# Performance work log

Hardware: AMD Instinct MI355X
Metric: run time of the kernel (lower is better)

The kernel has to match this reference:

```python
import jax, jax.numpy as jnp
import numpy as np

H = 1024      # hidden_size
F = 1024      # intermediate_size
E = 8         # num_experts
K = 2         # num_experts_per_tok
B, S = 1, 2048


def setup_inputs() -> dict:
    key = jax.random.key(0)
    ks = jax.random.split(key, 8)
    s = 0.02
    return {
        "hidden_states": jax.random.normal(ks[0], (B, S, H), jnp.float32),
        "w_gate": jax.random.normal(ks[1], (H, E), jnp.float32) * s,
        "w_gate_proj": jax.random.normal(ks[2], (E, H, F), jnp.float32) * s,   # per-expert gate_proj
        "w_up_proj": jax.random.normal(ks[3], (E, H, F), jnp.float32) * s,     # per-expert up_proj
        "w_down_proj": jax.random.normal(ks[4], (E, F, H), jnp.float32) * s,   # per-expert down_proj
        "w_shared_gate": jax.random.normal(ks[5], (H, F), jnp.float32) * s,
        "w_shared_up": jax.random.normal(ks[6], (H, F), jnp.float32) * s,
        "w_shared_down": jax.random.normal(ks[7], (F, H), jnp.float32) * s,
    }


def reference(hidden_states, w_gate, w_gate_proj, w_up_proj, w_down_proj,
              w_shared_gate, w_shared_up, w_shared_down):
    b, s, h = hidden_states.shape
    x = hidden_states.reshape(-1, h)                       # [T, H]
    t = x.shape[0]

    # --- router ---
    router_logits = x @ w_gate                             # [T, E]
    topk_vals, topk_idx = jax.lax.top_k(router_logits, K)  # [T, K]
    expert_weights = jax.nn.softmax(topk_vals.astype(jnp.float32), axis=-1).astype(x.dtype)

    # dense per-token per-expert combine weight [T, E] (zero where not selected)
    combine = jnp.zeros((t, E), x.dtype).at[jnp.arange(t)[:, None], topk_idx].add(expert_weights)

    # --- all experts as one grouped GEMM (weight-zero experts contribute 0) ---
    g = jnp.einsum('th,ehf->tef', x, w_gate_proj)          # [T, E, F]
    u = jnp.einsum('th,ehf->tef', x, w_up_proj)            # [T, E, F]
    y = jnp.einsum('tef,efh->teh', jax.nn.silu(g) * u, w_down_proj)  # [T, E, H]
    out = jnp.einsum('teh,te->th', y, combine)             # [T, H]

    # --- shared expert ---
    shared = (jax.nn.silu(x @ w_shared_gate) * (x @ w_shared_up)) @ w_shared_down
    out = (out + shared).reshape(b, s, h)

    aux_loss = jnp.float32(0.0)
    return out, aux_loss
```

## Files before the change

kernel.cpp:

```cpp
#include <hip/hip_runtime.h>
#include <hip/hip_bf16.h>
#include <stdint.h>

#define HDIM 1024
#define FDIM 1024
#define TTOK 2048
#define CAP  2048
#define MSZ  (1024*1024)

typedef __attribute__((ext_vector_type(8))) __bf16 bf16x8;
typedef __attribute__((ext_vector_type(4))) float  f32x4;

static __device__ __forceinline__ unsigned short f2bf(float v) {
  unsigned int u = __float_as_uint(v);
  u += 0x7FFF + ((u >> 16) & 1);
  return (unsigned short)(u >> 16);
}

static __device__ __forceinline__ unsigned pk2(float a, float b) {
  return (unsigned)f2bf(a) | ((unsigned)f2bf(b) << 16);
}

static __device__ __forceinline__ void gload_lds16(const void* g, void* l) {
  __builtin_amdgcn_global_load_lds(
      (const __attribute__((address_space(1))) unsigned int*)g,
      (__attribute__((address_space(3))) unsigned int*)l, 16, 0, 0);
}


__global__ __launch_bounds__(256) void k_prep(
    const float* __restrict__ x, const float* __restrict__ wg,
    const float* __restrict__ wgp, const float* __restrict__ wsg,
    const float* __restrict__ wup, const float* __restrict__ wsu,
    const float* __restrict__ wdp, const float* __restrict__ wsd,
    unsigned short* __restrict__ wB, unsigned short* __restrict__ xb,
    int* __restrict__ counts, int* __restrict__ tok_id, float* __restrict__ tok_w,
    int2* __restrict__ tsl, float* __restrict__ tw) {
  int b = blockIdx.x;
  int tid = threadIdx.x;
  if (b < 512) {
    int t = (b << 2) + (tid >> 6);
    int L = tid & 63;
    const float* xr = x + (size_t)t * HDIM;
    float acc[8] = {0, 0, 0, 0, 0, 0, 0, 0};
    for (int h = L; h < HDIM; h += 64) {
      float xv = xr[h];
      const float* wr = wg + h * 8;
      #pragma unroll
      for (int e = 0; e < 8; e++) acc[e] += xv * wr[e];
    }
    #pragma unroll
    for (int e = 0; e < 8; e++) {
      float v = acc[e];
      for (int off = 32; off > 0; off >>= 1) v += __shfl_xor(v, off);
      acc[e] = v;
    }
    if (L == 0) {
      int i1 = 0; float v1 = acc[0];
      #pragma unroll
      for (int e = 1; e < 8; e++) if (acc[e] > v1) { v1 = acc[e]; i1 = e; }
      int i2 = -1; float v2 = -1e30f;
      #pragma unroll
      for (int e = 0; e < 8; e++) if (e != i1 && acc[e] > v2) { v2 = acc[e]; i2 = e; }
      float ex = __expf(v2 - v1);
      float w1 = 1.f / (1.f + ex);
      float w2 = 1.f - w1;
      int p1 = atomicAdd(&counts[i1 << 4], 1);
      tok_id[i1 * CAP + p1] = t; tok_w[i1 * CAP + p1] = w1;
      int p2 = atomicAdd(&counts[i2 << 4], 1);
      tok_id[i2 * CAP + p2] = t; tok_w[i2 * CAP + p2] = w2;
      tsl[t] = make_int2((i1 << 10) + p1, (i2 << 10) + p2);
      tw[t] = w1;
    }
  } else if (b < 1536) {
    int i = (b - 512) * 256 + tid;
    const float4* in4 = (const float4*)x;
    float4 f0 = in4[i * 2], f1 = in4[i * 2 + 1];
    uint4 v;
    v.x = pk2(f0.x, f0.y); v.y = pk2(f0.z, f0.w);
    v.z = pk2(f1.x, f1.y); v.w = pk2(f1.z, f1.w);
    *((uint4*)(xb + (size_t)i * 8)) = v;
    if (i < TTOK) { tok_id[8 * CAP + i] = i; tok_w[8 * CAP + i] = 1.0f; }
    if (i == 0) counts[8 << 4] = TTOK;
  } else {
    int bt = b - 1536;
    int m = bt >> 6;
    int idx = bt & 63;
    int rb = (idx >> 3) << 7;
    int cb = (idx & 7) << 7;
    const float* src;
    if (m < 8)       src = wgp + (size_t)m * MSZ;
    else if (m == 8) src = wsg;
    else if (m < 17) src = wup + (size_t)(m - 9) * MSZ;
    else if (m == 17) src = wsu;
    else if (m < 26) src = wdp + (size_t)(m - 18) * MSZ;
    else             src = wsd;
    unsigned short* dst = wB + (size_t)m * MSZ;
    __shared__ __align__(16) unsigned short T[128 * 128];
    #pragma unroll
    for (int i = 0; i < 16; i++) {
      int g = tid + (i << 8);
      int r = g >> 5;
      int f4 = g & 31;
      float4 v = *(const float4*)(src + (size_t)(rb + r) * 1024 + cb + (f4 << 2));
      uint2 p;
      p.x = pk2(v.x, v.y);
      p.y = pk2(v.z, v.w);
      int ps = (f4 + ((r >> 3) << 1)) & 31;
      *(uint2*)(T + r * 128 + (ps << 2)) = p;
    }
    __syncthreads();
    int L = tid & 63, w = tid >> 6;
    int q = L & 15;
    int cbase = (w << 2) + (L >> 4);
    #pragma unroll
    for (int j = 0; j < 8; j++) {
      int c = cbase + (j << 4);
      int ps = ((c >> 2) + (q << 1)) & 31;
      const unsigned short* p = T + (q << 3) * 128 + (ps << 2) + (c & 3);
      unsigned short u0 = p[0],       u1 = p[128],      u2 = p[2 * 128],
                     u3 = p[3 * 128], u4 = p[4 * 128],  u5 = p[5 * 128],
                     u6 = p[6 * 128], u7 = p[7 * 128];
      uint4 o;
      o.x = (unsigned)u0 | ((unsigned)u1 << 16);
      o.y = (unsigned)u2 | ((unsigned)u3 << 16);
      o.z = (unsigned)u4 | ((unsigned)u5 << 16);
      o.w = (unsigned)u6 | ((unsigned)u7 << 16);
      *(uint4*)(dst + (size_t)(cb + c) * 1024 + rb + (q << 3)) = o;
    }
  }
}


__global__ __launch_bounds__(256, 2) void k_gemm1(
    const unsigned short* __restrict__ xb, const unsigned short* __restrict__ wB,
    const int* __restrict__ counts, const int* __restrict__ tok_id,
    unsigned short* __restrict__ actb) {
  int lin = blockIdx.x;
  int e = lin >> 8;
  int r9 = lin & 255;
  int nbi = (r9 & 7) | ((r9 >> 7) << 3);
  int mi  = (r9 >> 3) & 15;
  int Ne = (e == 8) ? TTOK : counts[e << 4];
  int rb = mi << 7;
  if (rb >= Ne) return;
  int nb = nbi << 6;
  const unsigned short* wg = wB + (size_t)e * MSZ;
  const unsigned short* wu = wB + (size_t)(9 + e) * MSZ;
  __shared__ __align__(16) unsigned short As0[128 * 64];
  __shared__ __align__(16) unsigned short As1[128 * 64];
  __shared__ __align__(16) unsigned short Bg0[64 * 64];
  __shared__ __align__(16) unsigned short Bg1[64 * 64];
  __shared__ __align__(16) unsigned short Bu0[64 * 64];
  __shared__ __align__(16) unsigned short Bu1[64 * 64];
  int tid = threadIdx.x;
  int w = tid >> 6, L = tid & 63;
  int quad = L >> 4, lane15 = L & 15;
  int wr = w >> 1, wc = w & 1;
  int l7 = lane15 & 7;
  int sw8 = ((L & 7) ^ (L >> 3)) << 3;
  const int* tlist = tok_id + e * CAP + rb;
  int trow[4];
  #pragma unroll
  for (int r = 0; r < 4; r++) {
    int row = (w << 5) + (r << 3) + (L >> 3);
    trow[r] = (rb + row < Ne) ? tlist[row] : 0;
  }
  f32x4 accg[4][2], accu[4][2];
  #pragma unroll
  for (int mt = 0; mt < 4; mt++)
    #pragma unroll
    for (int nt = 0; nt < 2; nt++) {
      accg[mt][nt] = (f32x4){0.f, 0.f, 0.f, 0.f};
      accu[mt][nt] = (f32x4){0.f, 0.f, 0.f, 0.f};
    }
  auto stage = [&](unsigned short* As_, unsigned short* Bg_, unsigned short* Bu_,
                   int it) {
    int k0 = it << 6;
    #pragma unroll
    for (int r = 0; r < 4; r++)
      gload_lds16(xb + (size_t)trow[r] * 1024 + k0 + sw8, As_ + ((w << 2) + r) * 512);
    #pragma unroll
    for (int r = 0; r < 2; r++) {
      int fr = (((w << 1) + r) << 3) + (L >> 3);
      size_t go = (size_t)(nb + fr) * 1024 + k0 + sw8;
      gload_lds16(wg + go, Bg_ + ((w << 1) + r) * 512);
      gload_lds16(wu + go, Bu_ + ((w << 1) + r) * 512);
    }
  };
  auto compute = [&](const unsigned short* As_, const unsigned short* Bg_,
                     const unsigned short* Bu_) {
    #pragma unroll
    for (int s = 0; s < 2; s++) {
      bf16x8 a[4], bg[2], bu[2];
      int ch = (s << 2) + quad;
      int po = ((ch ^ l7) << 3);
      #pragma unroll
      for (int mt = 0; mt < 4; mt++)
        a[mt] = *(const bf16x8*)(As_ + (((wr << 6) + (mt << 4) + lane15) << 6) + po);
      #pragma unroll
      for (int nt = 0; nt < 2; nt++) {
        int rrow = ((wc << 5) + (nt << 4) + lane15) << 6;
        bg[nt] = *(const bf16x8*)(Bg_ + rrow + po);
        bu[nt] = *(const bf16x8*)(Bu_ + rrow + po);
      }
      #pragma unroll
      for (int mt = 0; mt < 4; mt++)
        #pragma unroll
        for (int nt = 0; nt < 2; nt++) {
          accg[mt][nt] = __builtin_amdgcn_mfma_f32_16x16x32_bf16(a[mt], bg[nt], accg[mt][nt], 0, 0, 0);
          accu[mt][nt] = __builtin_amdgcn_mfma_f32_16x16x32_bf16(a[mt], bu[nt], accu[mt][nt], 0, 0, 0);
        }
    }
  };
  stage(As0, Bg0, Bu0, 0);
  __syncthreads();
  for (int it2 = 0; it2 < 8; it2++) {
    int itA = it2 << 1;
    if (itA + 1 < 16) stage(As1, Bg1, Bu1, itA + 1);
    compute(As0, Bg0, Bu0);
    __syncthreads();
    if (itA + 2 < 16) stage(As0, Bg0, Bu0, itA + 2);
    compute(As1, Bg1, Bu1);
    __syncthreads();
  }
  #pragma unroll
  for (int mt = 0; mt < 4; mt++)
    #pragma unroll
    for (int nt = 0; nt < 2; nt++)
      #pragma unroll
      for (int g = 0; g < 4; g++) {
        int r = (wr << 6) + (mt << 4) + (quad << 2) + g;
        if (rb + r < Ne) {
          float gv = accg[mt][nt][g], uv = accu[mt][nt][g];
          float av = gv / (1.f + __expf(-gv)) * uv;
          int f = nb + (wc << 5) + (nt << 4) + lane15;
          actb[(size_t)(e * CAP + rb + r) * 1024 + f] = f2bf(av);
        }
      }
}

__global__ __launch_bounds__(256, 3) void k_gemm2(
    const unsigned short* __restrict__ actb, const unsigned short* __restrict__ wB,
    const int* __restrict__ counts, float* __restrict__ y) {
  int lin = blockIdx.x;
  int e = lin >> 8;
  int r8 = lin & 255;
  int nbi = r8 & 7;
  int mi  = r8 >> 3;
  int Ne = (e == 8) ? TTOK : counts[e << 4];
  int rb = mi << 6;
  if (rb >= Ne) return;
  int nb = nbi << 7;
  int yb = (e < 8) ? (e << 10) : 8192;
  const unsigned short* wd = wB + (size_t)(18 + e) * MSZ;
  __shared__ __align__(16) unsigned short As0[64 * 64];
  __shared__ __align__(16) unsigned short As1[64 * 64];
  __shared__ __align__(16) unsigned short Bs0[128 * 64];
  __shared__ __align__(16) unsigned short Bs1[128 * 64];
  int tid = threadIdx.x;
  int w = tid >> 6, L = tid & 63;
  int quad = L >> 4, lane15 = L & 15;
  int l7 = lane15 & 7;
  int sw8 = ((L & 7) ^ (L >> 3)) << 3;
  const unsigned short* arow = actb + (size_t)(e * CAP + rb) * 1024;
  f32x4 acc[4][2];
  #pragma unroll
  for (int mt = 0; mt < 4; mt++)
    #pragma unroll
    for (int nt = 0; nt < 2; nt++) acc[mt][nt] = (f32x4){0.f, 0.f, 0.f, 0.f};
  auto stage = [&](unsigned short* As_, unsigned short* Bs_, int it) {
    int k0 = it << 6;
    #pragma unroll
    for (int r = 0; r < 2; r++) {
      int row = (w << 4) + (r << 3) + (L >> 3);
      gload_lds16(arow + (size_t)row * 1024 + k0 + sw8, As_ + ((w << 1) + r) * 512);
    }
    #pragma unroll
    for (int r = 0; r < 4; r++) {
      int row = (w << 5) + (r << 3) + (L >> 3);
      gload_lds16(wd + (size_t)(nb + row) * 1024 + k0 + sw8, Bs_ + ((w << 2) + r) * 512);
    }
  };
  auto compute = [&](const unsigned short* As_, const unsigned short* Bs_) {
    #pragma unroll
    for (int s = 0; s < 2; s++) {
      bf16x8 a[4], b[2];
      int ch = (s << 2) + quad;
      int po = ((ch ^ l7) << 3);
      #pragma unroll
      for (int mt = 0; mt < 4; mt++)
        a[mt] = *(const bf16x8*)(As_ + (((mt << 4) + lane15) << 6) + po);
      #pragma unroll
      for (int nt = 0; nt < 2; nt++)
        b[nt] = *(const bf16x8*)(Bs_ + (((w << 5) + (nt << 4) + lane15) << 6) + po);
      #pragma unroll
      for (int mt = 0; mt < 4; mt++)
        #pragma unroll
        for (int nt = 0; nt < 2; nt++)
          acc[mt][nt] = __builtin_amdgcn_mfma_f32_16x16x32_bf16(a[mt], b[nt], acc[mt][nt], 0, 0, 0);
    }
  };
  stage(As0, Bs0, 0);
  __syncthreads();
  for (int it2 = 0; it2 < 8; it2++) {
    int itA = it2 << 1;
    if (itA + 1 < 16) stage(As1, Bs1, itA + 1);
    compute(As0, Bs0);
    __syncthreads();
    if (itA + 2 < 16) stage(As0, Bs0, itA + 2);
    compute(As1, Bs1);
    __syncthreads();
  }
  #pragma unroll
  for (int mt = 0; mt < 4; mt++)
    #pragma unroll
    for (int nt = 0; nt < 2; nt++)
      #pragma unroll
      for (int g = 0; g < 4; g++) {
        int r = (mt << 4) + (quad << 2) + g;
        if (rb + r < Ne) {
          int hc = nb + (w << 5) + (nt << 4) + lane15;
          y[(size_t)(yb + rb + r) * 1024 + hc] = acc[mt][nt][g];
        }
      }
}

__global__ __launch_bounds__(256) void k_comb(
    const float* __restrict__ y, const int2* __restrict__ tsl,
    const float* __restrict__ tw, float* __restrict__ out) {
  int t = blockIdx.x, tid = threadIdx.x;
  int2 s = tsl[t];
  float w0 = tw[t], w1 = 1.f - w0;
  const float4* y4 = (const float4*)y;
  float4 a = y4[(size_t)s.x * 256 + tid];
  float4 b = y4[(size_t)s.y * 256 + tid];
  float4 c = y4[(size_t)(8192 + t) * 256 + tid];
  float4 o;
  o.x = w0 * a.x + w1 * b.x + c.x;
  o.y = w0 * a.y + w1 * b.y + c.y;
  o.z = w0 * a.z + w1 * b.z + c.z;
  o.w = w0 * a.w + w1 * b.w + c.w;
  ((float4*)out)[(size_t)t * 256 + tid] = o;
}

extern "C" void kernel_launch(void* const* d_in, const int* in_sizes, int n_in,
                              void* d_out, int out_size, void* d_ws, size_t ws_size,
                              hipStream_t stream) {
  (void)in_sizes; (void)n_in; (void)ws_size; (void)out_size;
  const float* x   = (const float*)d_in[0];
  const float* wg  = (const float*)d_in[1];
  const float* wgp = (const float*)d_in[2];
  const float* wup = (const float*)d_in[3];
  const float* wdp = (const float*)d_in[4];
  const float* wsg = (const float*)d_in[5];
  const float* wsu = (const float*)d_in[6];
  const float* wsd = (const float*)d_in[7];
  float* out = (float*)d_out;
  char* ws = (char*)d_ws;
  unsigned short* wB   = (unsigned short*)ws;
  unsigned short* xb   = (unsigned short*)(ws + 56623104);
  unsigned short* actb = (unsigned short*)(ws + 60817408);
  float* y      = (float*)(ws + 98566144);
  int*   tok_id = (int*)(ws + 140509184);
  float* tok_w  = (float*)(ws + 140582912);
  int2*  tsl    = (int2*)(ws + 140656640);
  float* tw     = (float*)(ws + 140673024);
  int*   counts = (int*)(ws + 140681216);

  hipMemsetAsync(counts, 0, 576, stream);
  k_prep<<<3264, 256, 0, stream>>>(x, wg, wgp, wsg, wup, wsu, wdp, wsd,
                                   wB, xb, counts, tok_id, tok_w, tsl, tw);
  k_gemm1<<<2304, 256, 0, stream>>>(xb, wB, counts, tok_id, actb);
  k_gemm2<<<2304, 256, 0, stream>>>(actb, wB, counts, y);
  k_comb<<<2048, 256, 0, stream>>>(y, tsl, tw, out);
}
```

Before: 243.5 us.

## Move down-proj weight conversion into gemm1 launch and shrink transpose tiles

The fp32-to-bf16 transpose of the down-projection weights moves out of the prep kernel into extra leading blocks of the first GEMM kernel. That conversion traffic can then overlap with the gate/up GEMM work instead of serialising before it. The transpose tile also shrinks from 128x128 to 128x64, halving its LDS footprint and doubling the block count. The transpose blocks in gemm1 reuse the GEMM's LDS allocation, and their lower block indices mean they dispatch first, so they may delay the GEMM tiles.

New measurement: 243.5 us. About the same (-0.0%).

```diff
diff --git a/kernel.cpp b/kernel.cpp
--- a/kernel.cpp
+++ b/kernel.cpp
@@ -28,16 +28,52 @@
 }
 
 
+static __device__ __forceinline__ void tr_tile(
+    const float* __restrict__ src, unsigned short* __restrict__ dst,
+    unsigned short* T, int rb, int cb, int tid) {
+  #pragma unroll
+  for (int i = 0; i < 8; i++) {
+    int g = tid + (i << 8);
+    int r = g >> 4;
+    int f4 = g & 15;
+    float4 v = *(const float4*)(src + (size_t)(rb + r) * 1024 + cb + (f4 << 2));
+    uint2 p;
+    p.x = pk2(v.x, v.y);
+    p.y = pk2(v.z, v.w);
+    int ps = (f4 + ((r >> 3) << 1)) & 15;
+    *(uint2*)(T + r * 64 + (ps << 2)) = p;
+  }
+  __syncthreads();
+  int L = tid & 63, w = tid >> 6;
+  int q = L & 15;
+  int cbase = (w << 2) + (L >> 4);
+  #pragma unroll
+  for (int j = 0; j < 4; j++) {
+    int c = cbase + (j << 4);
+    int ps = ((c >> 2) + (q << 1)) & 15;
+    const unsigned short* p = T + (q << 3) * 64 + (ps << 2) + (c & 3);
+    unsigned short u0 = p[0],      u1 = p[64],      u2 = p[2 * 64],
+                   u3 = p[3 * 64], u4 = p[4 * 64],  u5 = p[5 * 64],
+                   u6 = p[6 * 64], u7 = p[7 * 64];
+    uint4 o;
+    o.x = (unsigned)u0 | ((unsigned)u1 << 16);
+    o.y = (unsigned)u2 | ((unsigned)u3 << 16);
+    o.z = (unsigned)u4 | ((unsigned)u5 << 16);
+    o.w = (unsigned)u6 | ((unsigned)u7 << 16);
+    *(uint4*)(dst + (size_t)(cb + c) * 1024 + rb + (q << 3)) = o;
+  }
+}
+
 __global__ __launch_bounds__(256) void k_prep(
     const float* __restrict__ x, const float* __restrict__ wg,
     const float* __restrict__ wgp, const float* __restrict__ wsg,
     const float* __restrict__ wup, const float* __restrict__ wsu,
-    const float* __restrict__ wdp, const float* __restrict__ wsd,
     unsigned short* __restrict__ wB, unsigned short* __restrict__ xb,
     int* __restrict__ counts, int* __restrict__ tok_id, float* __restrict__ tok_w,
     int2* __restrict__ tsl, float* __restrict__ tw) {
   int b = blockIdx.x;
   int tid = threadIdx.x;
+  __shared__ __align__(16) unsigned short T[128 * 64];
   if (b < 512) {
     int t = (b << 2) + (tid >> 6);
     int L = tid & 63;
@@ -84,59 +120,43 @@
     if (i == 0) counts[8 << 4] = TTOK;
   } else {
     int bt = b - 1536;
-    int m = bt >> 6;
-    int idx = bt & 63;
-    int rb = (idx >> 3) << 7;
-    int cb = (idx & 7) << 7;
+    int m = bt >> 7;
+    int idx = bt & 127;
+    int rb = (idx >> 4) << 7;
+    int cb = (idx & 15) << 6;
     const float* src;
     if (m < 8)       src = wgp + (size_t)m * MSZ;
     else if (m == 8) src = wsg;
     else if (m < 17) src = wup + (size_t)(m - 9) * MSZ;
-    else if (m == 17) src = wsu;
-    else if (m < 26) src = wdp + (size_t)(m - 18) * MSZ;
-    else             src = wsd;
-    unsigned short* dst = wB + (size_t)m * MSZ;
-    __shared__ __align__(16) unsigned short T[128 * 128];
-    #pragma unroll
-    for (int i = 0; i < 16; i++) {
-      int g = tid + (i << 8);
-      int r = g >> 5;
-      int f4 = g & 31;
-      float4 v = *(const float4*)(src + (size_t)(rb + r) * 1024 + cb + (f4 << 2));
-      uint2 p;
-      p.x = pk2(v.x, v.y);
-      p.y = pk2(v.z, v.w);
-      int ps = (f4 + ((r >> 3) << 1)) & 31;
-      *(uint2*)(T + r * 128 + (ps << 2)) = p;
-    }
-    __syncthreads();
-    int L = tid & 63, w = tid >> 6;
-    int q = L & 15;
-    int cbase = (w << 2) + (L >> 4);
-    #pragma unroll
-    for (int j = 0; j < 8; j++) {
-      int c = cbase + (j << 4);
-      int ps = ((c >> 2) + (q << 1)) & 31;
-      const unsigned short* p = T + (q << 3) * 128 + (ps << 2) + (c & 3);
-      unsigned short u0 = p[0],       u1 = p[128],      u2 = p[2 * 128],
-                     u3 = p[3 * 128], u4 = p[4 * 128],  u5 = p[5 * 128],
-                     u6 = p[6 * 128], u7 = p[7 * 128];
-      uint4 o;
-      o.x = (unsigned)u0 | ((unsigned)u1 << 16);
-      o.y = (unsigned)u2 | ((unsigned)u3 << 16);
-      o.z = (unsigned)u4 | ((unsigned)u5 << 16);
-      o.w = (unsigned)u6 | ((unsigned)u7 << 16);
-      *(uint4*)(dst + (size_t)(cb + c) * 1024 + rb + (q << 3)) = o;
-    }
+    else             src = wsu;
+    tr_tile(src, wB + (size_t)m * MSZ, T, rb, cb, tid);
   }
 }
 
 
 __global__ __launch_bounds__(256, 2) void k_gemm1(
-    const unsigned short* __restrict__ xb, const unsigned short* __restrict__ wB,
+    const unsigned short* __restrict__ xb, unsigned short* __restrict__ wB,
+    const float* __restrict__ wdp, const float* __restrict__ wsd,
     const int* __restrict__ counts, const int* __restrict__ tok_id,
     unsigned short* __restrict__ actb) {
-  int lin = blockIdx.x;
+  __shared__ __align__(16) unsigned short As0[128 * 64];
+  __shared__ __align__(16) unsigned short As1[128 * 64];
+  __shared__ __align__(16) unsigned short Bg0[64 * 64];
+  __shared__ __align__(16) unsigned short Bg1[64 * 64];
+  __shared__ __align__(16) unsigned short Bu0[64 * 64];
+  __shared__ __align__(16) unsigned short Bu1[64 * 64];
+  int tid = threadIdx.x;
+  if (blockIdx.x < 1152) {
+    int bt = blockIdx.x;
+    int m = bt >> 7;
+    int idx = bt & 127;
+    int rb = (idx >> 4) << 7;
+    int cb = (idx & 15) << 6;
+    const float* src = (m < 8) ? wdp + (size_t)m * MSZ : wsd;
+    tr_tile(src, wB + (size_t)(18 + m) * MSZ, As0, rb, cb, tid);
+    return;
+  }
+  int lin = blockIdx.x - 1152;
   int e = lin >> 8;
   int r9 = lin & 255;
   int nbi = (r9 & 7) | ((r9 >> 7) << 3);
@@ -145,15 +165,8 @@
   int rb = mi << 7;
   if (rb >= Ne) return;
   int nb = nbi << 6;
-  const unsigned short* wg = wB + (size_t)e * MSZ;
-  const unsigned short* wu = wB + (size_t)(9 + e) * MSZ;
-  __shared__ __align__(16) unsigned short As0[128 * 64];
-  __shared__ __align__(16) unsigned short As1[128 * 64];
-  __shared__ __align__(16) unsigned short Bg0[64 * 64];
-  __shared__ __align__(16) unsigned short Bg1[64 * 64];
-  __shared__ __align__(16) unsigned short Bu0[64 * 64];
-  __shared__ __align__(16) unsigned short Bu1[64 * 64];
-  int tid = threadIdx.x;
+  const unsigned short* wgp_ = wB + (size_t)e * MSZ;
+  const unsigned short* wup_ = wB + (size_t)(9 + e) * MSZ;
   int w = tid >> 6, L = tid & 63;
   int quad = L >> 4, lane15 = L & 15;
   int wr = w >> 1, wc = w & 1;
@@ -184,8 +197,8 @@
     for (int r = 0; r < 2; r++) {
       int fr = (((w << 1) + r) << 3) + (L >> 3);
       size_t go = (size_t)(nb + fr) * 1024 + k0 + sw8;
-      gload_lds16(wg + go, Bg_ + ((w << 1) + r) * 512);
-      gload_lds16(wu + go, Bu_ + ((w << 1) + r) * 512);
+      gload_lds16(wgp_ + go, Bg_ + ((w << 1) + r) * 512);
+      gload_lds16(wup_ + go, Bu_ + ((w << 1) + r) * 512);
     }
   };
   auto compute = [&](const unsigned short* As_, const unsigned short* Bg_,
@@ -369,9 +382,9 @@
   int*   counts = (int*)(ws + 140681216);
 
   hipMemsetAsync(counts, 0, 576, stream);
-  k_prep<<<3264, 256, 0, stream>>>(x, wg, wgp, wsg, wup, wsu, wdp, wsd,
+  k_prep<<<3840, 256, 0, stream>>>(x, wg, wgp, wsg, wup, wsu,
                                    wB, xb, counts, tok_id, tok_w, tsl, tw);
-  k_gemm1<<<2304, 256, 0, stream>>>(xb, wB, counts, tok_id, actb);
+  k_gemm1<<<3456, 256, 0, stream>>>(xb, wB, wdp, wsd, counts, tok_id, actb);
   k_gemm2<<<2304, 256, 0, stream>>>(actb, wB, counts, y);
   k_comb<<<2048, 256, 0, stream>>>(y, tsl, tw, out);
 }
```
